# Kernel optimization log

Hardware: AMD Instinct MI355X
Metric: run time of the kernel (lower is better)

## Reference

```python
import jax, jax.numpy as jnp
import numpy as np

D_MODEL = 1024
HEADS = 16
HEAD_DIM = D_MODEL // HEADS


def setup_inputs() -> dict:
    key = jax.random.key(0)
    k1, k2 = jax.random.split(key)
    x = jax.random.normal(k1, (2, 2048, D_MODEL), dtype=jnp.float32)
    # nn.Linear(d_model, 3*d_model, bias=False): weight shape [3*d_model, d_model]
    W_qkv = jax.random.normal(k2, (3 * D_MODEL, D_MODEL), dtype=jnp.float32) * (D_MODEL ** -0.5)
    return {"x": x, "W_qkv": W_qkv}


def reference(x, W_qkv):
    b, t, c = x.shape
    qkv = jnp.einsum('btc,fc->btf', x, W_qkv)  # [b, t, 3c]
    q, k, v = jnp.split(qkv, 3, axis=-1)
    # [b, heads, t, head_dim]
    q = q.reshape(b, t, HEADS, HEAD_DIM).transpose(0, 2, 1, 3)
    k = k.reshape(b, t, HEADS, HEAD_DIM).transpose(0, 2, 1, 3)
    v = v.reshape(b, t, HEADS, HEAD_DIM).transpose(0, 2, 1, 3)
    scores = jnp.einsum('bhqd,bhkd->bhqk', q, k) * (HEAD_DIM ** -0.5)
    causal = jnp.tril(jnp.ones((t, t), dtype=bool))  # [t, t]
    scores = jnp.where(causal[None, None, :, :], scores, -jnp.inf)
    weights = jax.nn.softmax(scores, axis=-1)
    out = jnp.einsum('bhqk,bhkd->bhqd', weights, v)
    return out.transpose(0, 2, 1, 3).reshape(b, t, c)
```

## Files before the change

kernel.cpp:

```cpp
#include <hip/hip_runtime.h>
#include <hip/hip_bf16.h>
#include <stdint.h>

#define D_MODEL 1024
#define TOKENS  2048
#define HEADS   16
#define HDIM    64
#define NQKV    3072
#define MROWS   4096
#define SCALE   0.18033688011112042f

typedef __attribute__((ext_vector_type(4)))  float f32x4;
typedef __attribute__((ext_vector_type(16))) float f32x16;
typedef __attribute__((ext_vector_type(8)))  short bf16x8;

__device__ __forceinline__ unsigned short f2bf(float f) {
  union { float f; unsigned u; } v; v.f = f;
  unsigned u = v.u + 0x7FFFu + ((v.u >> 16) & 1u);
  return (unsigned short)(u >> 16);
}
__device__ __forceinline__ float bf2f(unsigned short b) {
  union { unsigned u; float f; } v; v.u = ((unsigned)b) << 16;
  return v.f;
}
__device__ __forceinline__ unsigned cvt_pk_bf16(float lo, float hi) {
  unsigned r;
  asm("v_cvt_pk_bf16_f32 %0, %1, %2" : "=v"(r) : "v"(lo), "v"(hi));
  return r;
}
__device__ __forceinline__ float xchg32(float v) {
  return __shfl_xor(v, 32);
}
__device__ __forceinline__ bf16x8 pfrag8(const float* g) {
  union { uint4 u; bf16x8 v; } r;
  r.u.x = cvt_pk_bf16(g[0], g[1]);
  r.u.y = cvt_pk_bf16(g[2], g[3]);
  r.u.z = cvt_pk_bf16(g[4], g[5]);
  r.u.w = cvt_pk_bf16(g[6], g[7]);
  return r.v;
}
__device__ __forceinline__ float max32t(const f32x16& a, const f32x16& b) {
  float t[16];
#pragma unroll
  for (int r = 0; r < 16; ++r) t[r] = fmaxf(a[r], b[r]);
#pragma unroll
  for (int s = 8; s > 0; s >>= 1)
#pragma unroll
    for (int r = 0; r < s; ++r) t[r] = fmaxf(t[r], t[r + s]);
  return t[0];
}
__device__ __forceinline__ float sum32t(const float* a, const float* b) {
  float t[16];
#pragma unroll
  for (int r = 0; r < 16; ++r) t[r] = a[r] + b[r];
#pragma unroll
  for (int s = 8; s > 0; s >>= 1)
#pragma unroll
    for (int r = 0; r < s; ++r) t[r] = t[r] + t[r + s];
  return t[0];
}

#define GLOAD16(g, l)                                                          \
  __builtin_amdgcn_global_load_lds(                                            \
      (const __attribute__((address_space(1))) unsigned int*)(g),              \
      (__attribute__((address_space(3))) unsigned int*)(l), 16, 0, 0)

__global__ __launch_bounds__(256) void cvt_bf16(const float* __restrict__ X,
                                                const float* __restrict__ W,
                                                unsigned short* __restrict__ Xb,
                                                unsigned short* __restrict__ Wb) {
  const size_t NX = (size_t)MROWS * D_MODEL;
  size_t i = ((size_t)blockIdx.x * 256 + threadIdx.x) * 8;
  const float* src; unsigned short* dst; size_t off;
  if (i < NX) { src = X; dst = Xb; off = i; }
  else        { src = W; dst = Wb; off = i - NX; }
  float4 a = ((const float4*)(src + off))[0];
  float4 b = ((const float4*)(src + off))[1];
  union { unsigned short s[8]; uint4 v; } u;
  u.s[0] = f2bf(a.x); u.s[1] = f2bf(a.y); u.s[2] = f2bf(a.z); u.s[3] = f2bf(a.w);
  u.s[4] = f2bf(b.x); u.s[5] = f2bf(b.y); u.s[6] = f2bf(b.z); u.s[7] = f2bf(b.w);
  *(uint4*)(dst + off) = u.v;
}

__global__ __launch_bounds__(256) void gemm_bf16(const unsigned short* __restrict__ A,
                                                 const unsigned short* __restrict__ B,
                                                 unsigned short* __restrict__ C) {
  __shared__ unsigned short sA[128 * 64];
  __shared__ unsigned short sB[128 * 64];
  const int tid  = threadIdx.x;
  const int lane = tid & 63;
  const int wave = tid >> 6;
  const int wr = wave >> 1, wc = wave & 1;
  const int row0 = blockIdx.x * 128;
  const int col0 = blockIdx.y * 128;

  f32x4 acc[4][4];
#pragma unroll
  for (int i = 0; i < 4; ++i)
#pragma unroll
    for (int j = 0; j < 4; ++j)
#pragma unroll
      for (int r = 0; r < 4; ++r) acc[i][j][r] = 0.f;

  const int lrow = lane & 15;
  const int lg   = lane >> 4;
  const int strow = (lane >> 3);
  const int stcol = (lane & 7) * 8;

#pragma unroll 1
  for (int k0 = 0; k0 < D_MODEL; k0 += 64) {
#pragma unroll
    for (int i = 0; i < 4; ++i) {
      const int r = wave * 32 + i * 8 + strow;
      GLOAD16(A + (size_t)(row0 + r) * D_MODEL + k0 + stcol, &sA[r * 64 + stcol]);
      GLOAD16(B + (size_t)(col0 + r) * D_MODEL + k0 + stcol, &sB[r * 64 + stcol]);
    }
    __syncthreads();

    bf16x8 av[4][2], bv[4][2];
#pragma unroll
    for (int c = 0; c < 2; ++c) {
#pragma unroll
      for (int i = 0; i < 4; ++i)
        av[i][c] = *(const bf16x8*)&sA[(wr * 64 + i * 16 + lrow) * 64 + c * 32 + lg * 8];
#pragma unroll
      for (int j = 0; j < 4; ++j)
        bv[j][c] = *(const bf16x8*)&sB[(wc * 64 + j * 16 + lrow) * 64 + c * 32 + lg * 8];
    }
#pragma unroll
    for (int c = 0; c < 2; ++c)
#pragma unroll
      for (int i = 0; i < 4; ++i)
#pragma unroll
        for (int j = 0; j < 4; ++j)
          acc[i][j] = __builtin_amdgcn_mfma_f32_16x16x32_bf16(av[i][c], bv[j][c], acc[i][j], 0, 0, 0);
    __syncthreads();
  }

  const int orow = row0 + wr * 64 + (lane >> 4) * 4;
  const int ocol = col0 + wc * 64 + (lane & 15);
#pragma unroll
  for (int i = 0; i < 4; ++i)
#pragma unroll
    for (int j = 0; j < 4; ++j)
#pragma unroll
      for (int r = 0; r < 4; ++r)
        C[(size_t)(orow + i * 16 + r) * NQKV + ocol + j * 16] = f2bf(acc[i][j][r]);
}

__global__ __launch_bounds__(256) void qkv_gemm(const float* __restrict__ X,
                                                const float* __restrict__ W,
                                                unsigned short* __restrict__ QKV) {
  __shared__ unsigned short sA[128 * 32];
  __shared__ unsigned short sB[128 * 32];
  const int tid  = threadIdx.x;
  const int lane = tid & 63;
  const int wave = tid >> 6;
  const int wr = wave >> 1, wc = wave & 1;
  const int row0 = blockIdx.x * 128;
  const int col0 = blockIdx.y * 128;

  f32x4 acc[4][4];
#pragma unroll
  for (int i = 0; i < 4; ++i)
#pragma unroll
    for (int j = 0; j < 4; ++j)
#pragma unroll
      for (int r = 0; r < 4; ++r) acc[i][j][r] = 0.f;

  const int srow = tid >> 1;
  const int scol = (tid & 1) * 16;
  union U16 { unsigned short s[8]; uint4 v; };

#pragma unroll 1
  for (int k0 = 0; k0 < D_MODEL; k0 += 32) {
    {
      const float* ga = X + (size_t)(row0 + srow) * D_MODEL + k0 + scol;
      const float* gb = W + (size_t)(col0 + srow) * D_MODEL + k0 + scol;
      float va[16], vb[16];
#pragma unroll
      for (int i = 0; i < 4; ++i) {
        float4 t = ((const float4*)ga)[i];
        va[4*i+0] = t.x; va[4*i+1] = t.y; va[4*i+2] = t.z; va[4*i+3] = t.w;
        float4 u = ((const float4*)gb)[i];
        vb[4*i+0] = u.x; vb[4*i+1] = u.y; vb[4*i+2] = u.z; vb[4*i+3] = u.w;
      }
      U16 ua0, ua1, ub0, ub1;
#pragma unroll
      for (int e = 0; e < 8; ++e) {
        ua0.s[e] = f2bf(va[e]);   ua1.s[e] = f2bf(va[8 + e]);
        ub0.s[e] = f2bf(vb[e]);   ub1.s[e] = f2bf(vb[8 + e]);
      }
      *(uint4*)&sA[srow * 32 + scol + 0] = ua0.v;
      *(uint4*)&sA[srow * 32 + scol + 8] = ua1.v;
      *(uint4*)&sB[srow * 32 + scol + 0] = ub0.v;
      *(uint4*)&sB[srow * 32 + scol + 8] = ub1.v;
    }
    __syncthreads();

    const int lrow = lane & 15;
    const int lk   = (lane >> 4) * 8;
    bf16x8 av[4], bv[4];
#pragma unroll
    for (int i = 0; i < 4; ++i)
      av[i] = *(const bf16x8*)&sA[(wr * 64 + i * 16 + lrow) * 32 + lk];
#pragma unroll
    for (int j = 0; j < 4; ++j)
      bv[j] = *(const bf16x8*)&sB[(wc * 64 + j * 16 + lrow) * 32 + lk];
#pragma unroll
    for (int i = 0; i < 4; ++i)
#pragma unroll
      for (int j = 0; j < 4; ++j)
        acc[i][j] = __builtin_amdgcn_mfma_f32_16x16x32_bf16(av[i], bv[j], acc[i][j], 0, 0, 0);
    __syncthreads();
  }

  const int orow = row0 + wr * 64 + (lane >> 4) * 4;
  const int ocol = col0 + wc * 64 + (lane & 15);
#pragma unroll
  for (int i = 0; i < 4; ++i)
#pragma unroll
    for (int j = 0; j < 4; ++j)
#pragma unroll
      for (int r = 0; r < 4; ++r)
        QKV[(size_t)(orow + i * 16 + r) * NQKV + ocol + j * 16] = f2bf(acc[i][j][r]);
}

__global__ __launch_bounds__(256, 2) void attn9(const unsigned short* __restrict__ QKV,
                                                float* __restrict__ Out) {
  __shared__ unsigned short sK [2][2][64 * 64];
  __shared__ unsigned short sVt[2][2][64 * 64];

  const int tid  = threadIdx.x;
  const int lane = tid & 63;
  const int wave = tid >> 6;
  const int l31  = lane & 31;
  const int hi   = lane >> 5;

  const int x = blockIdx.x;
  int bh, u;
  if (x < 256) { bh = x & 31; u = x >> 5; }
  else         { const int x2 = x - 256; bh = x2 & 31; u = 15 - (x2 >> 5); }

  const int b = bh >> 4, h = bh & 15;
  const int q0w  = u * 128 + wave * 32;
  const int qcol = q0w + l31;

  const unsigned short* Qbase = QKV + (size_t)(b * TOKENS) * NQKV + h * HDIM;
  const unsigned short* Kbase = Qbase + D_MODEL;
  const unsigned short* Vbase = Kbase + D_MODEL;

  bf16x8 qf[4];
  {
    const unsigned short* qrow = Qbase + (size_t)qcol * NQKV + hi * 8;
    union { unsigned short us[8]; bf16x8 v; ushort4 q[2]; } t;
#pragma unroll
    for (int dk = 0; dk < 4; ++dk) {
      t.q[0] = ((const ushort4*)(qrow + dk * 16))[0];
      t.q[1] = ((const ushort4*)(qrow + dk * 16))[1];
#pragma unroll
      for (int e = 0; e < 8; ++e) t.us[e] = f2bf(bf2f(t.us[e]) * SCALE);
      qf[dk] = t.v;
    }
  }

  f32x16 o0, o1;
#pragma unroll
  for (int r = 0; r < 16; ++r) { o0[r] = 0.f; o1[r] = 0.f; }
  float m = -1e30f, l = 0.f;

  const int vk0 = (tid & 15) * 4;
  const int vd0 = (tid >> 4) * 4;
  ushort4 va0, va1, va2, va3, vb0, vb1, vb2, vb3;

  const int lane16 = lane * 16;

#define KGLOAD(kt, buf, s)                                                     \
  {                                                                            \
    _Pragma("unroll")                                                          \
    for (int g = 0; g < 2; ++g) {                                              \
      const int base = g * 4096 + wave * 1024;                                 \
      const int d = base + lane16;                                             \
      const int row = d >> 7;                                                  \
      const int grow = (row & 51) | ((row & 4) << 1) | ((row & 8) >> 1);       \
      const int cb = (d & 127) ^ ((row & 7) << 4);                             \
      GLOAD16(Kbase + (size_t)((kt) * 64 + grow) * NQKV + (cb >> 1),           \
              (char*)&sK[buf][s][0] + base + lane16);                          \
    }                                                                          \
  }

#define VLOAD2(pp)                                                             \
  {                                                                            \
    const unsigned short* vsA = Vbase + (size_t)((2*(pp)) * 64 + vk0) * NQKV + vd0;   \
    va0 = *(const ushort4*)(vsA);                                              \
    va1 = *(const ushort4*)(vsA + NQKV);                                       \
    va2 = *(const ushort4*)(vsA + 2 * NQKV);                                   \
    va3 = *(const ushort4*)(vsA + 3 * NQKV);                                   \
    const unsigned short* vsB = Vbase + (size_t)((2*(pp)+1) * 64 + vk0) * NQKV + vd0; \
    vb0 = *(const ushort4*)(vsB);                                              \
    vb1 = *(const ushort4*)(vsB + NQKV);                                       \
    vb2 = *(const ushort4*)(vsB + 2 * NQKV);                                   \
    vb3 = *(const ushort4*)(vsB + 3 * NQKV);                                   \
  }

#define VWRITE1(buf, s, t0, t1, t2, t3)                                        \
  {                                                                            \
    ushort4 c0, c1, c2, c3;                                                    \
    c0.x = t0.x; c0.y = t1.x; c0.z = t2.x; c0.w = t3.x;                        \
    c1.x = t0.y; c1.y = t1.y; c1.z = t2.y; c1.w = t3.y;                        \
    c2.x = t0.z; c2.y = t1.z; c2.z = t2.z; c2.w = t3.z;                        \
    c3.x = t0.w; c3.y = t1.w; c3.z = t2.w; c3.w = t3.w;                        \
    char* dV = (char*)&sVt[buf][s][0];                                         \
    _Pragma("unroll")                                                          \
    for (int e = 0; e < 4; ++e) {                                              \
      const int dim = vd0 + e;                                                 \
      const int o2 = (dim * 128 + vk0 * 2) ^ ((dim & 7) << 4);                 \
      ushort4 cc = (e == 0) ? c0 : (e == 1) ? c1 : (e == 2) ? c2 : c3;         \
      *(ushort4*)(dV + o2) = cc;                                               \
    }                                                                          \
  }

#define QKT(cK, rowbase, st)                                                   \
  {                                                                            \
    _Pragma("unroll")                                                          \
    for (int dk = 0; dk < 4; ++dk) {                                           \
      const int row = (rowbase);                                               \
      bf16x8 kf = *(const bf16x8*)((cK) + ((row * 128 + hi * 16 + dk * 32) ^ ((row & 7) << 4))); \
      st = __builtin_amdgcn_mfma_f32_32x32x16_bf16(kf, qf[dk], st, 0, 0, 0);   \
    }                                                                          \
  }

#define PV4(cV, bpX, bpY, koff)                                                \
  {                                                                            \
    const int r0 = l31, r1 = l31 + 32;                                         \
    bf16x8 vf;                                                                 \
    vf = *(const bf16x8*)((cV) + ((r0 * 128 + hi * 16 + (koff)) ^ ((r0 & 7) << 4)));      \
    o0 = __builtin_amdgcn_mfma_f32_32x32x16_bf16(vf, bpX, o0, 0, 0, 0);        \
    vf = *(const bf16x8*)((cV) + ((r1 * 128 + hi * 16 + (koff)) ^ ((r1 & 7) << 4)));      \
    o1 = __builtin_amdgcn_mfma_f32_32x32x16_bf16(vf, bpX, o1, 0, 0, 0);        \
    vf = *(const bf16x8*)((cV) + ((r0 * 128 + hi * 16 + (koff) + 32) ^ ((r0 & 7) << 4))); \
    o0 = __builtin_amdgcn_mfma_f32_32x32x16_bf16(vf, bpY, o0, 0, 0, 0);        \
    vf = *(const bf16x8*)((cV) + ((r1 * 128 + hi * 16 + (koff) + 32) ^ ((r1 & 7) << 4))); \
    o1 = __builtin_amdgcn_mfma_f32_32x32x16_bf16(vf, bpY, o1, 0, 0, 0);        \
  }

  KGLOAD(0, 0, 0);
  KGLOAD(1, 0, 1);
  VLOAD2(0);
  VWRITE1(0, 0, va0, va1, va2, va3);
  VWRITE1(0, 1, vb0, vb1, vb2, vb3);
  __syncthreads();

#pragma unroll 1
  for (int p = 0; p < u; ++p) {
    const int cur = p & 1;
    KGLOAD(2 * (p + 1),     cur ^ 1, 0);
    KGLOAD(2 * (p + 1) + 1, cur ^ 1, 1);
    VLOAD2(p + 1);

    const char* cKA = (const char*)&sK[cur][0][0];
    const char* cKB = (const char*)&sK[cur][1][0];
    const char* cVA = (const char*)&sVt[cur][0][0];
    const char* cVB = (const char*)&sVt[cur][1][0];

    f32x16 sA0, sA1, sB0, sB1;
#pragma unroll
    for (int r = 0; r < 16; ++r) { sA0[r] = 0.f; sA1[r] = 0.f; sB0[r] = 0.f; sB1[r] = 0.f; }

    QKT(cKA, l31,      sA0);
    QKT(cKA, l31 + 32, sA1);
    QKT(cKB, l31,      sB0);
    QKT(cKB, l31 + 32, sB1);

    {
      float mx = max32t(sA0, sA1);
      mx = fmaxf(mx, xchg32(mx));
      if (!__all(mx - m <= 8.f)) {
        const float mnew = fmaxf(m, mx);
        const float corr = exp2f(m - mnew);
        m = mnew;
        l *= corr;
#pragma unroll
        for (int r = 0; r < 16; ++r) { o0[r] *= corr; o1[r] *= corr; }
      }
      float pA0[16], pA1[16];
#pragma unroll
      for (int r = 0; r < 16; ++r) { pA0[r] = exp2f(sA0[r] - m); pA1[r] = exp2f(sA1[r] - m); }
      float ps = sum32t(pA0, pA1);
      ps += xchg32(ps);
      l += ps;
      bf16x8 a0 = pfrag8(&pA0[0]), a1 = pfrag8(&pA0[8]);
      bf16x8 a2 = pfrag8(&pA1[0]), a3 = pfrag8(&pA1[8]);
      PV4(cVA, a0, a1, 0);
      PV4(cVA, a2, a3, 64);
    }

    {
      float mx = max32t(sB0, sB1);
      mx = fmaxf(mx, xchg32(mx));
      if (!__all(mx - m <= 8.f)) {
        const float mnew = fmaxf(m, mx);
        const float corr = exp2f(m - mnew);
        m = mnew;
        l *= corr;
#pragma unroll
        for (int r = 0; r < 16; ++r) { o0[r] *= corr; o1[r] *= corr; }
      }
      float pB0[16], pB1[16];
#pragma unroll
      for (int r = 0; r < 16; ++r) { pB0[r] = exp2f(sB0[r] - m); pB1[r] = exp2f(sB1[r] - m); }
      float ps = sum32t(pB0, pB1);
      ps += xchg32(ps);
      l += ps;
      bf16x8 b0 = pfrag8(&pB0[0]), b1 = pfrag8(&pB0[8]);
      bf16x8 b2 = pfrag8(&pB1[0]), b3 = pfrag8(&pB1[8]);
      PV4(cVB, b0, b1, 0);
      PV4(cVB, b2, b3, 64);
    }

    VWRITE1(cur ^ 1, 0, va0, va1, va2, va3);
    VWRITE1(cur ^ 1, 1, vb0, vb1, vb2, vb3);
    __syncthreads();
  }

  {
    const int cur = u & 1;
    const char* cK[2] = { (const char*)&sK[cur][0][0], (const char*)&sK[cur][1][0] };
    const char* cV[2] = { (const char*)&sVt[cur][0][0], (const char*)&sVt[cur][1][0] };
    const int nsub = (wave >= 2) ? 2 : 1;
#pragma unroll 1
    for (int s = 0; s < nsub; ++s) {
      const int kbase = u * 128 + s * 64;
      const bool diag  = (wave >= 2) ? (s == 1) : true;
      const bool do_hi = diag ? ((wave & 1) == 1) : true;

      f32x16 st0, st1;
#pragma unroll
      for (int r = 0; r < 16; ++r) { st0[r] = 0.f; st1[r] = 0.f; }

      QKT(cK[s], l31, st0);
      if (do_hi) QKT(cK[s], l31 + 32, st1);

      if (diag) {
#pragma unroll
        for (int r = 0; r < 16; ++r) {
          const int key0 = kbase + (r & 7) + ((r & 8) << 1) + 8 * hi;
          if (key0 > qcol) st0[r] = -1e30f;
          if (do_hi && key0 + 32 > qcol) st1[r] = -1e30f;
        }
      }

      float mx = do_hi ? max32t(st0, st1) : max32t(st0, st0);
      mx = fmaxf(mx, xchg32(mx));

      if (!__all(mx - m <= 8.f)) {
        const float mnew = fmaxf(m, mx);
        const float corr = exp2f(m - mnew);
        m = mnew;
        l *= corr;
#pragma unroll
        for (int r = 0; r < 16; ++r) { o0[r] *= corr; o1[r] *= corr; }
      }

      float p0[16], p1[16];
#pragma unroll
      for (int r = 0; r < 16; ++r) p0[r] = exp2f(st0[r] - m);
      float ps;
      if (do_hi) {
#pragma unroll
        for (int r = 0; r < 16; ++r) p1[r] = exp2f(st1[r] - m);
        ps = sum32t(p0, p1);
      } else {
        float z[16];
#pragma unroll
        for (int r = 0; r < 16; ++r) z[r] = 0.f;
        ps = sum32t(p0, z);
      }
      ps += xchg32(ps);
      l += ps;

      bf16x8 c0 = pfrag8(&p0[0]), c1 = pfrag8(&p0[8]);
      PV4(cV[s], c0, c1, 0);
      if (do_hi) {
        bf16x8 c2 = pfrag8(&p1[0]), c3 = pfrag8(&p1[8]);
        PV4(cV[s], c2, c3, 64);
      }
    }
  }

  {
    const float inv = 1.f / l;
    float* orow = Out + (size_t)(b * TOKENS + qcol) * D_MODEL + h * HDIM;
#pragma unroll
    for (int g = 0; g < 4; ++g) {
      float4 w0, w1;
      w0.x = o0[4*g+0] * inv; w0.y = o0[4*g+1] * inv;
      w0.z = o0[4*g+2] * inv; w0.w = o0[4*g+3] * inv;
      w1.x = o1[4*g+0] * inv; w1.y = o1[4*g+1] * inv;
      w1.z = o1[4*g+2] * inv; w1.w = o1[4*g+3] * inv;
      *(float4*)(orow + 8 * g + 4 * hi)      = w0;
      *(float4*)(orow + 8 * g + 4 * hi + 32) = w1;
    }
  }
}

extern "C" void kernel_launch(void* const* d_in, const int* in_sizes, int n_in,
                              void* d_out, int out_size, void* d_ws, size_t ws_size,
                              hipStream_t stream) {
  const float* X = (const float*)d_in[0];
  const float* W = (const float*)d_in[1];
  float* Out = (float*)d_out;
  unsigned short* QKV = (unsigned short*)d_ws;

  const size_t QKV_E = (size_t)MROWS * NQKV;
  const size_t XB_E  = (size_t)MROWS * D_MODEL;
  const size_t WB_E  = (size_t)NQKV * D_MODEL;
  const size_t need_bf16 = (QKV_E + XB_E + WB_E) * 2;

  if (ws_size >= need_bf16) {
    unsigned short* Xb = QKV + QKV_E;
    unsigned short* Wb = Xb + XB_E;
    cvt_bf16<<<(XB_E + WB_E) / (256 * 8), 256, 0, stream>>>(X, W, Xb, Wb);
    gemm_bf16<<<dim3(MROWS / 128, NQKV / 128), 256, 0, stream>>>(Xb, Wb, QKV);
  } else {
    qkv_gemm<<<dim3(MROWS / 128, NQKV / 128), 256, 0, stream>>>(X, W, QKV);
  }

  attn9<<<512, 256, 0, stream>>>(QKV, Out);
}
```

Baseline: 109.6 us.

## Replace bf16 QKV GEMM with 256x256 double-buffered 8-wave pipelined kernel

Swaps the 128x128 single-buffered bf16 GEMM for a 256x256-tile kernel run by 512 threads. It double-buffers LDS, with swizzled layout, and interleaves global-to-LDS staging of the next k-tile with MFMA phases on quarter tiles, using explicit waitcnt, barriers and setprio. The goal is to hide global load latency, cut LDS bank conflicts and raise arithmetic intensity per block. The cost is only 192 blocks on a 256-CU part and heavy register and LDS use at one block per CU.

```diff
diff --git a/kernel.cpp b/kernel.cpp
--- a/kernel.cpp
+++ b/kernel.cpp
@@ -82,70 +82,123 @@
   *(uint4*)(dst + off) = u.v;
 }
 
-__global__ __launch_bounds__(256) void gemm_bf16(const unsigned short* __restrict__ A,
-                                                 const unsigned short* __restrict__ B,
-                                                 unsigned short* __restrict__ C) {
-  __shared__ unsigned short sA[128 * 64];
-  __shared__ unsigned short sB[128 * 64];
+__global__ __launch_bounds__(512, 1) void gemm8(const unsigned short* __restrict__ A,
+                                                const unsigned short* __restrict__ B,
+                                                unsigned short* __restrict__ C) {
+  __shared__ unsigned short sA[2][2][128][64];
+  __shared__ unsigned short sB[2][2][128][64];
+
   const int tid  = threadIdx.x;
   const int lane = tid & 63;
   const int wave = tid >> 6;
-  const int wr = wave >> 1, wc = wave & 1;
-  const int row0 = blockIdx.x * 128;
-  const int col0 = blockIdx.y * 128;
-
-  f32x4 acc[4][4];
-#pragma unroll
-  for (int i = 0; i < 4; ++i)
+  const int wr   = wave >> 2;
+  const int wc   = wave & 3;
+  const int l15  = lane & 15;
+  const int lg   = lane >> 4;
+
+  const int bm = blockIdx.x;
+  const int bn = blockIdx.y;
+
+  f32x4 acc[8][4];
+#pragma unroll
+  for (int i = 0; i < 8; ++i)
 #pragma unroll
     for (int j = 0; j < 4; ++j)
 #pragma unroll
       for (int r = 0; r < 4; ++r) acc[i][j][r] = 0.f;
 
-  const int lrow = lane & 15;
-  const int lg   = lane >> 4;
-  const int strow = (lane >> 3);
-  const int stcol = (lane & 7) * 8;
+  const int srow = tid >> 3;
+  const int scb  = (tid & 7) * 16;
+  const int ssce = (scb ^ ((srow & 4) << 3)) >> 1;
+
+  const unsigned short* Ag = A + (size_t)(bm * 256) * D_MODEL;
+  const unsigned short* Bg = B + (size_t)(bn * 256) * D_MODEL;
+
+#define STG_A(buf, hf, t)                                                      \
+  { GLOAD16(Ag + (size_t)((hf) * 128 + srow) * D_MODEL + (t) * 64 + ssce,      \
+            (char*)&sA[buf][hf][0][0] + srow * 128 + scb);                     \
+    GLOAD16(Ag + (size_t)((hf) * 128 + 64 + srow) * D_MODEL + (t) * 64 + ssce, \
+            (char*)&sA[buf][hf][0][0] + 8192 + srow * 128 + scb); }
+#define STG_B(buf, hf, t)                                                      \
+  { GLOAD16(Bg + (size_t)((hf) * 128 + srow) * D_MODEL + (t) * 64 + ssce,      \
+            (char*)&sB[buf][hf][0][0] + srow * 128 + scb);                     \
+    GLOAD16(Bg + (size_t)((hf) * 128 + 64 + srow) * D_MODEL + (t) * 64 + ssce, \
+            (char*)&sB[buf][hf][0][0] + 8192 + srow * 128 + scb); }
+
+  const char* aBse[2] = { (const char*)&sA[0][wr][0][0], (const char*)&sA[1][wr][0][0] };
+  const char* bBse[2] = { (const char*)&sB[0][wc >> 1][0][0], (const char*)&sB[1][wc >> 1][0][0] };
+  const int swzl = (l15 & 4) << 3;
+  const int cbs0 = (lg * 16) ^ swzl;
+  const int cbs1 = (64 + lg * 16) ^ swzl;
+  const int arow = l15 * 128;
+  const int brow = ((wc & 1) * 64 + l15) * 128;
+
+#define DO_PHASE(qm, qn, buf, STAGE_STMT, DO_VM)                               \
+  {                                                                            \
+    bf16x8 a_[4][2], b_[2][2];                                                 \
+    _Pragma("unroll")                                                          \
+    for (int i = 0; i < 4; ++i) {                                              \
+      a_[i][0] = *(const bf16x8*)(aBse[buf] + ((qm)*4 + i) * 2048 + arow + cbs0); \
+      a_[i][1] = *(const bf16x8*)(aBse[buf] + ((qm)*4 + i) * 2048 + arow + cbs1); \
+    }                                                                          \
+    _Pragma("unroll")                                                          \
+    for (int n = 0; n < 2; ++n) {                                              \
+      b_[n][0] = *(const bf16x8*)(bBse[buf] + ((qn)*2 + n) * 2048 + brow + cbs0); \
+      b_[n][1] = *(const bf16x8*)(bBse[buf] + ((qn)*2 + n) * 2048 + brow + cbs1); \
+    }                                                                          \
+    STAGE_STMT;                                                                \
+    if (DO_VM) asm volatile("s_waitcnt vmcnt(2)" ::: "memory");                \
+    __builtin_amdgcn_s_barrier();                                              \
+    asm volatile("s_waitcnt lgkmcnt(0)" ::: "memory");                         \
+    __builtin_amdgcn_sched_barrier(0);                                         \
+    __builtin_amdgcn_s_setprio(1);                                             \
+    _Pragma("unroll")                                                          \
+    for (int ks = 0; ks < 2; ++ks)                                             \
+      _Pragma("unroll")                                                        \
+      for (int i = 0; i < 4; ++i)                                              \
+        _Pragma("unroll")                                                      \
+        for (int n = 0; n < 2; ++n)                                            \
+          acc[(qm)*4 + i][(qn)*2 + n] = __builtin_amdgcn_mfma_f32_16x16x32_bf16( \
+              a_[i][ks], b_[n][ks], acc[(qm)*4 + i][(qn)*2 + n], 0, 0, 0);     \
+    __builtin_amdgcn_s_setprio(0);                                             \
+    __builtin_amdgcn_s_barrier();                                              \
+  }
+
+  STG_A(0, 0, 0);
+  STG_B(0, 0, 0);
+  STG_A(0, 1, 0);
+  STG_B(0, 1, 0);
+  STG_B(1, 0, 1);
+  asm volatile("s_waitcnt vmcnt(2)" ::: "memory");
+  __builtin_amdgcn_s_barrier();
 
 #pragma unroll 1
-  for (int k0 = 0; k0 < D_MODEL; k0 += 64) {
-#pragma unroll
-    for (int i = 0; i < 4; ++i) {
-      const int r = wave * 32 + i * 8 + strow;
-      GLOAD16(A + (size_t)(row0 + r) * D_MODEL + k0 + stcol, &sA[r * 64 + stcol]);
-      GLOAD16(B + (size_t)(col0 + r) * D_MODEL + k0 + stcol, &sB[r * 64 + stcol]);
-    }
-    __syncthreads();
-
-    bf16x8 av[4][2], bv[4][2];
-#pragma unroll
-    for (int c = 0; c < 2; ++c) {
-#pragma unroll
-      for (int i = 0; i < 4; ++i)
-        av[i][c] = *(const bf16x8*)&sA[(wr * 64 + i * 16 + lrow) * 64 + c * 32 + lg * 8];
-#pragma unroll
-      for (int j = 0; j < 4; ++j)
-        bv[j][c] = *(const bf16x8*)&sB[(wc * 64 + j * 16 + lrow) * 64 + c * 32 + lg * 8];
-    }
-#pragma unroll
-    for (int c = 0; c < 2; ++c)
-#pragma unroll
-      for (int i = 0; i < 4; ++i)
-#pragma unroll
-        for (int j = 0; j < 4; ++j)
-          acc[i][j] = __builtin_amdgcn_mfma_f32_16x16x32_bf16(av[i][c], bv[j][c], acc[i][j], 0, 0, 0);
-    __syncthreads();
-  }
-
-  const int orow = row0 + wr * 64 + (lane >> 4) * 4;
-  const int ocol = col0 + wc * 64 + (lane & 15);
-#pragma unroll
-  for (int i = 0; i < 4; ++i)
-#pragma unroll
-    for (int j = 0; j < 4; ++j)
+  for (int j = 0; j < 8; ++j) {
+    const int t1 = 2 * j + 1;
+    const int t2 = 2 * j + 2;
+    const int t3 = 2 * j + 3;
+    DO_PHASE(0, 0, 0, { STG_A(1, 0, t1); }, 0);
+    DO_PHASE(1, 0, 0, { STG_A(1, 1, t1); }, 0);
+    DO_PHASE(0, 1, 0, { STG_B(1, 1, t1); }, 0);
+    DO_PHASE(1, 1, 0, { if (t2 < 16) STG_B(0, 0, t2); }, 1);
+    DO_PHASE(0, 0, 1, { if (t2 < 16) STG_A(0, 0, t2); }, 0);
+    DO_PHASE(1, 0, 1, { if (t2 < 16) STG_A(0, 1, t2); }, 0);
+    DO_PHASE(0, 1, 1, { if (t2 < 16) STG_B(0, 1, t2); }, 0);
+    DO_PHASE(1, 1, 1, { if (t3 < 16) STG_B(1, 0, t3); }, 1);
+  }
+
+  const int orow0 = bm * 256 + wr * 128 + lg * 4;
+  const int ocol0 = bn * 256 + wc * 64 + l15;
+#pragma unroll
+  for (int mi = 0; mi < 8; ++mi)
+#pragma unroll
+    for (int ni = 0; ni < 4; ++ni)
 #pragma unroll
       for (int r = 0; r < 4; ++r)
-        C[(size_t)(orow + i * 16 + r) * NQKV + ocol + j * 16] = f2bf(acc[i][j][r]);
+        C[(size_t)(orow0 + mi * 16 + r) * NQKV + ocol0 + ni * 16] = f2bf(acc[mi][ni][r]);
+#undef STG_A
+#undef STG_B
+#undef DO_PHASE
 }
 
 __global__ __launch_bounds__(256) void qkv_gemm(const float* __restrict__ X,
@@ -521,7 +574,7 @@
     unsigned short* Xb = QKV + QKV_E;
     unsigned short* Wb = Xb + XB_E;
     cvt_bf16<<<(XB_E + WB_E) / (256 * 8), 256, 0, stream>>>(X, W, Xb, Wb);
-    gemm_bf16<<<dim3(MROWS / 128, NQKV / 128), 256, 0, stream>>>(Xb, Wb, QKV);
+    gemm8<<<dim3(MROWS / 256, NQKV / 256), 512, 0, stream>>>(Xb, Wb, QKV);
   } else {
     qkv_gemm<<<dim3(MROWS / 128, NQKV / 128), 256, 0, stream>>>(X, W, QKV);
   }
```

Measured after the change: 110.1 us. No clear change (+0.4%).
